# Kernel tuning notes

Measured on AMD Instinct MI355X. Metric: run time of the kernel, lower is better.

The kernel has to match this reference:

```python
import jax, jax.numpy as jnp
import numpy as np
from jax.scipy.linalg import solve_triangular

REG = 1e-3  # DCDicL regularization hyperparameter


def _p2o(psf, H, W):
    # point-spread-function -> optical transfer function: zero-pad to (H,W),
    # circularly shift so kernel center sits at origin, then rfft2.
    ds = psf.shape[-1]
    otf = jnp.zeros(psf.shape[:-2] + (H, W), psf.dtype)
    otf = otf.at[..., :ds, :ds].set(psf)
    otf = jnp.roll(otf, (-(ds // 2), -(ds // 2)), axis=(-2, -1))
    return jnp.fft.rfft2(otf)


def _solve_fft(X, D, Y, alpha, H, W):
    # X:(N,1,Cin,H,Wf)  D:(N,Cout,Cin,H,Wf)  Y:(N,Cout,1,H,Wf)  complex64
    C_in = X.shape[2]
    a = (alpha / C_in)[..., None]              # (N,1,1,1,1) real scalar per sample
    Dc = jnp.conj(D)
    Z = Y * D + a * X                          # (N,Cout,Cin,H,Wf)
    factor1 = Z / a
    num = jnp.sum(Dc * Z, axis=2, keepdims=True)
    den = a * jnp.sum(Dc * D, axis=2, keepdims=True) + a * a  # csum: real add
    factor2 = D * (num / den)
    Xn = jnp.mean(factor1 - factor2, axis=1)   # (N,Cin,H,Wf)
    return jnp.fft.irfft2(Xn, s=(H, W))


def _solve_ls(x, d, y, alpha, reg):
    # x:(N,Cin,H,W)  d:(N,Cout,Cin,ds,ds)  y:(N,Cout,H,W)
    N, C_in, H, W = x.shape
    C_out, ds = d.shape[1], d.shape[-1]
    P = ds - 1
    M = C_in * ds * ds
    dn = ('NCHW', 'OIHW', 'NCHW')

    # All-pairs full cross-correlation (torch cal_xtx via sample-wise conv3d):
    # corr[n,i,o,u,v] = sum_{h,w} x[n,i,h+u-P,w+v-P] * x[n,o,h,w]
    def pair_corr(xn):
        return jax.lax.conv_general_dilated(xn[:, None], xn[:, None], (1, 1),
                                            [(P, P), (P, P)], dimension_numbers=dn)
    corr = jax.vmap(pair_corr)(x)              # (N, i, o, 2P+1, 2P+1)

    # Block-Toeplitz Gram (replaces unfold/flip/index-permute copies):
    # Q[n,(o,k1,k2),(i,q1,q2)] = corr[n,i,o, P+q1-k1, P+q2-k2]
    r = jnp.arange(ds)
    off = P + r[None, :] - r[:, None]          # (k, q)
    Q6 = corr[:, :, :, off[:, :, None, None], off[None, None, :, :]]  # (N,i,o,k1,q1,k2,q2)
    Q = jnp.transpose(Q6, (0, 2, 3, 5, 1, 4, 6)).reshape(N, M, M)

    # cal_xty: 'same'-padded correlation of x with y
    p = (ds - 1) // 2
    def xty_corr(xn, yn):
        return jax.lax.conv_general_dilated(xn[:, None], yn[:, None], (1, 1),
                                            [(p, p), (p, p)], dimension_numbers=dn)
    xty = jax.vmap(xty_corr)(x, y)             # (N, i, Cout, ds, ds)
    Pm = jnp.transpose(xty, (0, 1, 3, 4, 2)).reshape(N, M, C_out)

    a = (alpha * (H * W) * reg / (ds * ds * C_in)).reshape(N, 1, 1)
    Q = Q + a * jnp.eye(M, dtype=Q.dtype)
    Pm = Pm + a * jnp.transpose(d.reshape(N, C_out, M), (0, 2, 1))

    L = jnp.linalg.cholesky(Q)
    Zs = solve_triangular(L, Pm, lower=True)
    Dm = solve_triangular(jnp.swapaxes(L, -1, -2), Zs, lower=False)
    return jnp.transpose(Dm.reshape(N, C_in, ds, ds, C_out), (0, 4, 1, 2, 3))


def _forward(x, d, y, alpha_x, alpha_d, reg):
    H, W = x.shape[-2], x.shape[-1]
    X = jnp.fft.rfft2(x)[:, None]              # (N,1,Cin,H,Wf)
    D = _p2o(d, H, W)                          # (N,Cout,Cin,H,Wf)
    Y = jnp.fft.rfft2(y)[:, :, None]           # (N,Cout,1,H,Wf)
    x_new = _solve_fft(X, D, Y, alpha_x, H, W)
    d_new = _solve_ls(x_new, d, y, alpha_d, reg)
    return x_new, d_new


def setup_inputs() -> dict:
    key = jax.random.key(0)
    k0, k1, k2 = jax.random.split(key, 3)
    x = jax.random.normal(k0, (4, 64, 128, 128), jnp.float32)
    d = jax.random.normal(k1, (4, 1, 64, 5, 5), jnp.float32)
    y = jax.random.normal(k2, (4, 1, 128, 128), jnp.float32)
    alpha_x = jnp.ones((4, 1, 1, 1), jnp.float32)
    alpha_d = jnp.ones((4, 1, 1, 1), jnp.float32)
    reg = jnp.float32(REG)
    return {"x": x, "d": d, "y": y, "alpha_x": alpha_x, "alpha_d": alpha_d, "reg": reg}


def reference(x, d, y, alpha_x, alpha_d, reg):
    return _forward(x, d, y, alpha_x, alpha_d, reg)
```

## Files before the change

kernel.cpp:

```cpp
#include <hip/hip_runtime.h>
#include <hip/hip_bf16.h>
#include <math.h>

#define PI_F 3.14159265358979323846f

#define NS   4
#define CIN  64
#define HH   128
#define WW   128
#define KXN  65
#define NPIX (HH*WW)
#define MMAT 1600
#define NIT  6
#define SD   136
#define SLAB 167936

#define OFF_SINV 0
#define OFF_E    33280
#define OFF_ER   98816
#define OFF_VR   231936
#define OFF_WB   298496
#define OFF_R    364032
#define OFF_RP   1691136
#define OFF_EP   1691136
#define OFF_PP   1691136
#define OFF_XB   7196160
#define XB0C     4734976
#define OFF_DV   0
#define OFF_RV   6400
#define OFF_PV   12800
#define OFF_AP   19200
#define OFF_RV2  25600
#define OFF_PAPP 32000

#define WRED(x) { (x)+=__shfl_down((x),32); (x)+=__shfl_down((x),16); (x)+=__shfl_down((x),8); \
                  (x)+=__shfl_down((x),4);  (x)+=__shfl_down((x),2);  (x)+=__shfl_down((x),1); }

typedef __attribute__((ext_vector_type(8))) short bf16x8;
typedef __attribute__((ext_vector_type(4))) float f32x4;

__global__ __launch_bounds__(256) void k_sinv(const float* __restrict__ dict,
                                              const float* __restrict__ alpha_x,
                                              float* __restrict__ ws) {
  int idx = blockIdx.x * 256 + threadIdx.x;
  int n = blockIdx.y;
  if (idx >= HH * KXN) return;
  int ky = idx / KXN, kx = idx % KXN;
  float tr[25], ti[25];
  {
    float eyr[5], eyi[5], exr[5], exi[5];
#pragma unroll
    for (int a = 0; a < 5; ++a) {
      float s, c;
      sincosf(-2.0f * PI_F * (float)(ky * (a - 2)) / 128.0f, &s, &c);
      eyr[a] = c; eyi[a] = s;
      sincosf(-2.0f * PI_F * (float)(kx * (a - 2)) / 128.0f, &s, &c);
      exr[a] = c; exi[a] = s;
    }
#pragma unroll
    for (int a = 0; a < 5; ++a)
#pragma unroll
      for (int b = 0; b < 5; ++b) {
        tr[a*5+b] = eyr[a]*exr[b] - eyi[a]*exi[b];
        ti[a*5+b] = eyr[a]*exi[b] + eyi[a]*exr[b];
      }
  }
  const float* dn = dict + n * CIN * 25;
  float S = 0.0f;
  for (int c = 0; c < CIN; ++c) {
    const float* p = dn + c * 25;
    float Dr = 0.0f, Di = 0.0f;
#pragma unroll
    for (int t = 0; t < 25; ++t) { Dr += p[t]*tr[t]; Di += p[t]*ti[t]; }
    S += Dr*Dr + Di*Di;
  }
  float a = alpha_x[n] * (1.0f/64.0f);
  ws[OFF_SINV + (n*HH + ky)*KXN + kx] = 1.0f / (S + a);
}

__global__ __launch_bounds__(256) void k_e(const float* __restrict__ x,
                                           const float* __restrict__ dict,
                                           float* __restrict__ ws) {
  __shared__ __align__(16) float xs[68*SD];
  __shared__ float psf_s[25];
  int c = blockIdx.x, n = blockIdx.y, hh = blockIdx.z;
  int tid = threadIdx.x;
  if (tid < 25) psf_s[tid] = dict[(n*CIN + c)*25 + tid];
  const float* Xc = x + (size_t)(n*CIN + c)*NPIX;
  int rbase = hh*64 - 2;
  for (int k = tid; k < 68*132; k += 256) {
    int R = k / 132, C = k - R*132;
    int gh = (rbase + R) & 127;
    int gw = (C - 2) & 127;
    xs[R*SD + C] = Xc[gh*128 + gw];
  }
  __syncthreads();
  int cs = tid & 31, rs = tid >> 5;
  int c0 = cs*4, r0 = rs*8;
  float w[5][8];
#pragma unroll
  for (int k = 0; k < 4; ++k) {
    f32x4 a = *(const f32x4*)&xs[(r0+k)*SD + c0];
    f32x4 b = *(const f32x4*)&xs[(r0+k)*SD + c0 + 4];
#pragma unroll
    for (int e = 0; e < 4; ++e) { w[k][e] = a[e]; w[k][4+e] = b[e]; }
  }
  float* EPo = ws + OFF_EP + (size_t)(c*4 + n)*NPIX + (size_t)(hh*64 + r0)*128 + c0;
#pragma unroll
  for (int row = 0; row < 8; ++row) {
    int slot = (row + 4) % 5;
    f32x4 a = *(const f32x4*)&xs[(r0+row+4)*SD + c0];
    f32x4 b = *(const f32x4*)&xs[(r0+row+4)*SD + c0 + 4];
#pragma unroll
    for (int e = 0; e < 4; ++e) { w[slot][e] = a[e]; w[slot][4+e] = b[e]; }
    f32x4 acc = (f32x4){0.f,0.f,0.f,0.f};
#pragma unroll
    for (int u = 0; u < 5; ++u)
#pragma unroll
      for (int v = 0; v < 5; ++v) {
        float pv = psf_s[u*5 + v];
#pragma unroll
        for (int p = 0; p < 4; ++p)
          acc[p] += pv * w[(row+u) % 5][p+v];
      }
    *(f32x4*)(EPo + (size_t)row*128) = acc;
  }
}

__global__ __launch_bounds__(256) void k_e2(const float* __restrict__ y,
                                            float* __restrict__ ws) {
  int n = blockIdx.y;
  int p = blockIdx.x*256 + threadIdx.x;
  float s = 0.0f;
#pragma unroll 8
  for (int c = 0; c < CIN; ++c) s += ws[OFF_EP + (size_t)(c*4 + n)*NPIX + p];
  ws[OFF_E + n*NPIX + p] = y[n*NPIX + p] - s;
}

__global__ __launch_bounds__(256) void k_fft_rows(float* __restrict__ ws) {
  __shared__ float twr[128], twi[128];
  int tid = threadIdx.x;
  if (tid < 128) { float s, c; sincosf(-2.0f*PI_F*(float)tid/128.0f, &s, &c); twr[tid]=c; twi[tid]=s; }
  __syncthreads();
  int idx = blockIdx.x*256 + tid, n = blockIdx.y;
  if (idx >= HH*KXN) return;
  int h = idx / KXN, k = idx % KXN;
  const float* row = ws + OFF_E + (n*HH + h)*WW;
  float sr = 0, si = 0;
  for (int w = 0; w < 128; ++w) {
    int t = (w*k) & 127;
    float v = row[w];
    sr += v*twr[t]; si += v*twi[t];
  }
  float* o = ws + OFF_ER + ((n*HH + h)*KXN + k)*2;
  o[0] = sr; o[1] = si;
}

__global__ __launch_bounds__(128) void k_fft_colpipe(float* __restrict__ ws) {
  __shared__ float twr[128], twi[128];
  __shared__ float ecr[128], eci[128];
  __shared__ float ewr[128], ewi[128];
  int tid = threadIdx.x;
  int kx = blockIdx.x, n = blockIdx.y;
  { float s, c; sincosf(-2.0f*PI_F*(float)tid/128.0f, &s, &c); twr[tid]=c; twi[tid]=s; }
  const float* Er = ws + OFF_ER + (size_t)n*HH*KXN*2;
  ecr[tid] = Er[(tid*KXN + kx)*2];
  eci[tid] = Er[(tid*KXN + kx)*2 + 1];
  __syncthreads();
  {
    int ky = tid;
    float sr = 0, si = 0;
    for (int h = 0; h < 128; ++h) {
      int t = (h*ky) & 127;
      float ar = ecr[h], ai = eci[h];
      sr += ar*twr[t] - ai*twi[t];
      si += ar*twi[t] + ai*twr[t];
    }
    float sv = ws[OFF_SINV + (n*HH + ky)*KXN + kx];
    ewr[ky] = sr*sv; ewi[ky] = si*sv;
  }
  __syncthreads();
  {
    int h = tid;
    float sr = 0, si = 0;
    for (int ky = 0; ky < 128; ++ky) {
      int t = (h*ky) & 127;
      float ar = ewr[ky], ai = ewi[ky];
      sr += ar*twr[t] + ai*twi[t];
      si += ai*twr[t] - ar*twi[t];
    }
    float* o = ws + OFF_VR + ((n*HH + h)*KXN + kx)*2;
    o[0] = sr; o[1] = si;
  }
}

__global__ __launch_bounds__(256) void k_ifft_rows(float* __restrict__ ws) {
  __shared__ float twr[128], twi[128];
  int tid = threadIdx.x;
  if (tid < 128) { float s, c; sincosf(-2.0f*PI_F*(float)tid/128.0f, &s, &c); twr[tid]=c; twi[tid]=s; }
  __syncthreads();
  int idx = blockIdx.x*256 + tid, n = blockIdx.y;
  int h = idx >> 7, w = idx & 127;
  const float* Vr = ws + OFF_VR + (size_t)n*HH*KXN*2;
  float s = 0.0f;
  for (int kx = 0; kx <= 64; ++kx) {
    int t = (w*kx) & 127;
    float ar = Vr[(h*KXN + kx)*2], ai = Vr[(h*KXN + kx)*2 + 1];
    float re = ar*twr[t] + ai*twi[t];
    s += (kx == 0 || kx == 64) ? re : 2.0f*re;
  }
  ws[OFF_WB + (n*HH + h)*WW + w] = s * (1.0f/16384.0f);
}

__global__ __launch_bounds__(256) void k_xnew(const float* __restrict__ x,
                                              const float* __restrict__ dict,
                                              const float* __restrict__ ws,
                                              float* __restrict__ out) {
  __shared__ float psf_s[CIN*25];
  __shared__ float wt[20*20];
  int n = blockIdx.y, tile = blockIdx.x, tid = threadIdx.x;
  int h0 = (tile >> 3) * 16, w0 = (tile & 7) * 16;
  for (int i = tid; i < CIN*25; i += 256) psf_s[i] = dict[n*CIN*25 + i];
  for (int i = tid; i < 400; i += 256) {
    int r = i / 20, cc = i % 20;
    int gh = (h0 + r - 2) & 127, gw = (w0 + cc - 2) & 127;
    wt[i] = ws[OFF_WB + (n*HH + gh)*WW + gw];
  }
  __syncthreads();
  int py = tid >> 4, px = tid & 15;
  int h = h0+py, w = w0+px;
  for (int c = 0; c < CIN; ++c) {
    float acc = 0.0f;
    const float* pp = psf_s + c*25;
#pragma unroll
    for (int a = 0; a < 5; ++a)
#pragma unroll
      for (int b = 0; b < 5; ++b)
        acc += pp[a*5+b] * wt[(py + 4 - a)*20 + (px + 4 - b)];
    int gi = ((n*CIN + c)*HH + h)*WW + w;
    out[gi] = x[gi] + acc;
  }
}

__global__ __launch_bounds__(256) void k_pad(const float* __restrict__ xn,
                                             float* __restrict__ ws) {
  ushort* xb0 = (ushort*)(ws + OFF_XB);
  ushort* xb1 = xb0 + XB0C;
  int ch = blockIdx.y;
  int idx = blockIdx.x*256 + threadIdx.x;
  if (ch == 0 && idx == 0) xb1[0] = 0;
  if (idx >= 136*136) return;
  int hp = idx / 136, wp = idx % 136;
  float v = 0.0f;
  if (hp >= 4 && hp < 132 && wp >= 4 && wp < 132)
    v = xn[(size_t)ch*NPIX + (hp-4)*128 + (wp-4)];
  __hip_bfloat16 b = __float2bfloat16(v);
  ushort bits = *(ushort*)&b;
  size_t o = (size_t)ch*18496 + idx;
  xb0[o] = bits;
  xb1[o + 1] = bits;
}

__global__ __launch_bounds__(256, 3) void k_gemm(float* __restrict__ ws) {
  __shared__ __align__(16) ushort sA0[64*128];
  __shared__ __align__(16) ushort sA1[64*128];
  __shared__ __align__(16) ushort sB [64*128];

  const ushort* xb0 = (const ushort*)(ws + OFF_XB);
  const ushort* xb1 = xb0 + XB0C;
  int fid = blockIdx.x;
  int xcd = fid & 7, l = fid >> 3;
  int nn = xcd & 3, hi = xcd >> 2;
  int g = l % 21, m = l / 21;
  int sl = m*2 + hi;

  int tid = threadIdx.x;
  int wv = tid >> 6, lane = tid & 63;
  int l16 = lane & 15, quad = lane >> 4;
  int lr = lane >> 4, lc = lane & 15;

  int sidx0 = 2*g;
  int sidx1 = 2*g + 1;
  int sval1 = (sidx1 <= 40);
  if (sidx1 > 40) sidx1 = 40;
  int uv0 = sidx0 + 40, uv1 = sidx1 + 40;
  int u0 = uv0 / 9, v0 = uv0 % 9;
  int u1 = uv1 / 9, v1 = uv1 % 9;

  size_t chanBase = (size_t)(nn*64) * 18496;
  int ridx0 = sl * 16;
  const ushort* pB  = xb0 + chanBase + 548 + (size_t)ridx0*136;
  size_t a0e = chanBase + (size_t)(u0 + ridx0)*136 + v0;
  size_t a1e = chanBase + (size_t)(u1 + ridx0)*136 + v1;
  const ushort* pA0 = (v0 & 1) ? (xb1 + a0e + 1) : (xb0 + a0e);
  const ushort* pA1 = (v1 & 1) ? (xb1 + a1e + 1) : (xb0 + a1e);

  f32x4 acc[2][4];
#pragma unroll
  for (int s = 0; s < 2; ++s)
#pragma unroll
    for (int jt = 0; jt < 4; ++jt) acc[s][jt] = (f32x4){0.f,0.f,0.f,0.f};

  for (int r = 0; r < 16; ++r) {
    if (r) __syncthreads();
#pragma unroll
    for (int c = 0; c < 4; ++c) {
      int row = wv*16 + c*4 + lr;
      int sw = ((lc ^ (row & 15)) * 8);
      size_t goff = (size_t)row * 18496 + (size_t)lc * 8;
      {
        const uint2* p = (const uint2*)(pB + goff);
        uint2 b0 = p[0], b1 = p[1];
        *(uint2*)&sB[row*128 + sw]     = b0;
        *(uint2*)&sB[row*128 + sw + 4] = b1;
      }
      {
        const uint* p = (const uint*)(pA0 + goff);
        uint4 v4; v4.x = p[0]; v4.y = p[1]; v4.z = p[2]; v4.w = p[3];
        *(uint4*)&sA0[row*128 + sw] = v4;
      }
      {
        const uint* p = (const uint*)(pA1 + goff);
        uint4 v4; v4.x = p[0]; v4.y = p[1]; v4.z = p[2]; v4.w = p[3];
        *(uint4*)&sA1[row*128 + sw] = v4;
      }
    }
    __syncthreads();
#pragma unroll
    for (int kt = 0; kt < 4; ++kt) {
      int c16 = kt*4 + quad;
      int sw = ((c16 ^ l16) * 8);
      bf16x8 af0 = *(const bf16x8*)&sA0[(wv*16 + l16)*128 + sw];
      bf16x8 af1 = *(const bf16x8*)&sA1[(wv*16 + l16)*128 + sw];
      bf16x8 bf[4];
#pragma unroll
      for (int jt = 0; jt < 4; ++jt)
        bf[jt] = *(const bf16x8*)&sB[(jt*16 + l16)*128 + sw];
#pragma unroll
      for (int jt = 0; jt < 4; ++jt) {
        acc[0][jt] = __builtin_amdgcn_mfma_f32_16x16x32_bf16(af0, bf[jt], acc[0][jt], 0, 0, 0);
        acc[1][jt] = __builtin_amdgcn_mfma_f32_16x16x32_bf16(af1, bf[jt], acc[1][jt], 0, 0, 0);
      }
    }
    pB += 136; pA0 += 136; pA1 += 136;
  }

  int io = wv*16 + quad*4;
  {
    float* dst = ws + OFF_RP + (((size_t)nn*8 + sl)*41 + sidx0)*4096;
#pragma unroll
    for (int jt = 0; jt < 4; ++jt) {
      int jout = jt*16 + l16;
      *reinterpret_cast<f32x4*>(dst + jout*64 + io) = acc[0][jt];
    }
  }
  if (sval1) {
    float* dst = ws + OFF_RP + (((size_t)nn*8 + sl)*41 + sidx1)*4096;
#pragma unroll
    for (int jt = 0; jt < 4; ++jt) {
      int jout = jt*16 + l16;
      *reinterpret_cast<f32x4*>(dst + jout*64 + io) = acc[1][jt];
    }
  }
}

__global__ __launch_bounds__(256) void k_rsumtrans(float* __restrict__ ws) {
  __shared__ float tile[64][65];
  int s = blockIdx.x, n = blockIdx.y;
  float* base0 = ws + OFF_RP + ((size_t)n*8)*SLAB + (size_t)s*4096;
  int t = threadIdx.x;
#pragma unroll
  for (int p = 0; p < 4; ++p) {
    int vidx = p*256 + t;
    int row = vidx >> 4, c0 = (vidx & 15)*4;
    f32x4 sum = (f32x4){0.f,0.f,0.f,0.f};
#pragma unroll
    for (int sl = 0; sl < 8; ++sl)
      sum += *(const f32x4*)(base0 + (size_t)sl*SLAB + row*64 + c0);
    *(f32x4*)(base0 + row*64 + c0) = sum;
    tile[row][c0]   = sum[0]; tile[row][c0+1] = sum[1];
    tile[row][c0+2] = sum[2]; tile[row][c0+3] = sum[3];
  }
  __syncthreads();
  float* PT = base0 + SLAB;
#pragma unroll
  for (int p = 0; p < 4; ++p) {
    int vidx = p*256 + t;
    int row = vidx >> 4, c0 = (vidx & 15)*4;
    f32x4 o;
#pragma unroll
    for (int e = 0; e < 4; ++e) o[e] = tile[c0+e][row];
    *(f32x4*)(PT + row*64 + c0) = o;
  }
}

__global__ __launch_bounds__(256) void k_rmerge(float* __restrict__ ws) {
  __shared__ float ld[81][65];
  int i = blockIdx.x, n = blockIdx.y;
  const float* P  = ws + OFF_RP + ((size_t)n*8 + 0)*SLAB;
  const float* PT = ws + OFF_RP + ((size_t)n*8 + 1)*SLAB;
  int t = threadIdx.x;
  for (int k = t; k < 81*64; k += 256) {
    int uv = k >> 6, j = k & 63;
    float v = (uv >= 40) ? PT[(size_t)(uv-40)*4096 + i*64 + j]
                         : P [(size_t)(40-uv)*4096 + i*64 + j];
    ld[uv][j] = v;
  }
  __syncthreads();
  float* out = ws + OFF_R + ((size_t)(n*64 + i)*64)*81;
  for (int k = t; k < 64*81; k += 256) {
    int j = k / 81, uv = k - j*81;
    out[k] = ld[uv][j];
  }
}

__global__ __launch_bounds__(256) void k_pm(const float* __restrict__ xn,
                                            const float* __restrict__ y,
                                            float* __restrict__ ws) {
  __shared__ __align__(16) float xs[68*SD];
  __shared__ float red_s[4][25];
  int i = blockIdx.x, n = blockIdx.y, hh = blockIdx.z;
  int tid = threadIdx.x;
  const float* Xi = xn + (size_t)(n*CIN + i)*NPIX;
  int rbase = hh*64 - 2;
  for (int k = tid; k < 68*132; k += 256) {
    int R = k / 132, C = k - R*132;
    int hr = rbase + R, wc = C - 2;
    float v = 0.0f;
    if (hr >= 0 && hr < 128 && wc >= 0 && wc < 128) v = Xi[hr*128 + wc];
    xs[R*SD + C] = v;
  }
  __syncthreads();
  int cs = tid & 31, rs = tid >> 5;
  int c0 = cs*4, r0 = rs*8;
  float w[5][8];
#pragma unroll
  for (int k = 0; k < 4; ++k) {
    f32x4 a = *(const f32x4*)&xs[(r0+k)*SD + c0];
    f32x4 b = *(const f32x4*)&xs[(r0+k)*SD + c0 + 4];
#pragma unroll
    for (int e = 0; e < 4; ++e) { w[k][e] = a[e]; w[k][4+e] = b[e]; }
  }
  float acc[25];
#pragma unroll
  for (int t = 0; t < 25; ++t) acc[t] = 0.0f;
  const float* yp = y + (size_t)n*NPIX + (size_t)(hh*64 + r0)*128 + c0;
#pragma unroll
  for (int row = 0; row < 8; ++row) {
    int slot = (row + 4) % 5;
    f32x4 a = *(const f32x4*)&xs[(r0+row+4)*SD + c0];
    f32x4 b = *(const f32x4*)&xs[(r0+row+4)*SD + c0 + 4];
#pragma unroll
    for (int e = 0; e < 4; ++e) { w[slot][e] = a[e]; w[slot][4+e] = b[e]; }
    f32x4 yv = *(const f32x4*)(yp + (size_t)row*128);
#pragma unroll
    for (int u = 0; u < 5; ++u)
#pragma unroll
      for (int v = 0; v < 5; ++v) {
#pragma unroll
        for (int p = 0; p < 4; ++p)
          acc[u*5+v] += w[(row+u) % 5][p+v] * yv[p];
      }
  }
  int lane = tid & 63, wv = tid >> 6;
#pragma unroll
  for (int t = 0; t < 25; ++t) {
    float v = acc[t];
    WRED(v);
    if (lane == 0) red_s[wv][t] = v;
  }
  __syncthreads();
  if (tid < 25) {
    float s = red_s[0][tid] + red_s[1][tid] + red_s[2][tid] + red_s[3][tid];
    ws[OFF_PP + ((size_t)(hh*4 + n)*64 + i)*25 + tid] = s;
  }
}

__global__ __launch_bounds__(64) void k_pm2(const float* __restrict__ dict,
                                            const float* __restrict__ alpha_d,
                                            const float* __restrict__ regp,
                                            float* __restrict__ ws) {
  int i = blockIdx.x, n = blockIdx.y, t = threadIdx.x;
  if (t >= 25) return;
  float s = 0.0f;
#pragma unroll
  for (int tg = 0; tg < 2; ++tg) s += ws[OFF_PP + ((size_t)(tg*4 + n)*64 + i)*25 + t];
  float ad = alpha_d[n] * 16384.0f * regp[0] * (1.0f/1600.0f);
  float val = s + ad * dict[(n*CIN + i)*25 + t];
  int idx = n*MMAT + i*25 + t;
  ws[OFF_RV + idx] = val;
  ws[OFF_PV + idx] = val;
}

__global__ __launch_bounds__(256) void k_cg_first(float* __restrict__ ws,
                                                  const float* __restrict__ alpha_d,
                                                  const float* __restrict__ regp) {
  __shared__ float vv[MMAT];
  __shared__ float part[25][66];
  int n = blockIdx.y, j = blockIdx.x, tid = threadIdx.x;
  for (int t = tid; t < MMAT; t += 256) vv[t] = ws[OFF_PV + n*MMAT + t];
  __syncthreads();
  int i = tid & 63, qq = tid >> 6;
  const float* Rij = ws + OFF_R + (((size_t)n*CIN + i)*CIN + j)*81;
  const float* vi = &vv[i*25];
#pragma unroll
  for (int s6 = 0; s6 < 7; ++s6) {
    int ac = qq + 4*s6;
    if (ac < 25) {
      int a = ac/5, c = ac%5;
      float s = 0.0f;
#pragma unroll
      for (int b = 0; b < 5; ++b)
#pragma unroll
        for (int d = 0; d < 5; ++d)
          s += Rij[(4+b-a)*9 + (4+d-c)] * vi[b*5+d];
      part[ac][i] = s;
    }
  }
  __syncthreads();
  float contrib = 0.0f;
  if (tid < 25) {
    float s = 0.0f;
    for (int t = 0; t < 64; ++t) s += part[tid][t];
    float reg = alpha_d[n] * 16384.0f * regp[0] * (1.0f/1600.0f);
    s += reg * vv[j*25 + tid];
    ws[OFF_AP + n*MMAT + j*25 + tid] = s;
    contrib = s * vv[j*25 + tid];
  }
  if (tid < 64) {
    WRED(contrib);
    if (tid == 0) ws[OFF_PAPP + 0*256 + n*64 + j] = contrib;
  }
}

__global__ __launch_bounds__(256) void k_cg_step(float* __restrict__ ws, int it,
                                                 int last, float* __restrict__ out,
                                                 const float* __restrict__ alpha_d,
                                                 const float* __restrict__ regp) {
  __shared__ float vv[MMAT];
  __shared__ float red_s[9];
  __shared__ float part[25][66];
  int n = blockIdx.y, j = blockIdx.x, tid = threadIdx.x;
  const float* rsrc = ws + ((it & 1) ? OFF_RV2 : OFF_RV) + n*MMAT;
  float*       rdst = ws + ((it & 1) ? OFF_RV  : OFF_RV2) + n*MMAT;
  int lane = tid & 63, wvi = tid >> 6;

  float rold[7], apv[7];
  float rrp = 0.0f;
#pragma unroll
  for (int t = 0; t < 7; ++t) {
    int idx = tid + 256*t;
    rold[t] = 0.0f; apv[t] = 0.0f;
    if (idx < MMAT) {
      rold[t] = rsrc[idx];
      apv[t]  = ws[OFF_AP + n*MMAT + idx];
      rrp += rold[t]*rold[t];
    }
  }
  WRED(rrp);
  if (lane == 0) red_s[wvi] = rrp;
  float pp = (tid < 64) ? ws[OFF_PAPP + it*256 + n*64 + tid] : 0.0f;
  if (tid < 64) { WRED(pp); if (tid == 0) red_s[4] = pp; }
  __syncthreads();
  float rr_old = red_s[0] + red_s[1] + red_s[2] + red_s[3];
  float alpha = rr_old / (red_s[4] + 1e-30f);

  if (last) {
    if (tid < 25) {
      int idx = n*MMAT + j*25 + tid;
      float dv = ws[OFF_DV + idx] + alpha * ws[OFF_PV + idx];
      out[4194304 + n*MMAT + j*25 + tid] = dv;
    }
    return;
  }

  float rrnp = 0.0f;
#pragma unroll
  for (int t = 0; t < 7; ++t) {
    int idx = tid + 256*t;
    if (idx < MMAT) {
      float rn = rold[t] - alpha * apv[t];
      vv[idx] = rn;
      rrnp += rn*rn;
    }
  }
  WRED(rrnp);
  __syncthreads();
  if (lane == 0) red_s[5 + wvi] = rrnp;
  __syncthreads();
  float rr_new = red_s[5] + red_s[6] + red_s[7] + red_s[8];
  float beta = rr_new / (rr_old + 1e-30f);

  int i = tid & 63, qq = tid >> 6;
  const float* Rij = ws + OFF_R + (((size_t)n*CIN + i)*CIN + j)*81;
  const float* vi = &vv[i*25];
#pragma unroll
  for (int s6 = 0; s6 < 7; ++s6) {
    int ac = qq + 4*s6;
    if (ac < 25) {
      int a = ac/5, c = ac%5;
      float s = 0.0f;
#pragma unroll
      for (int b = 0; b < 5; ++b)
#pragma unroll
        for (int d = 0; d < 5; ++d)
          s += Rij[(4+b-a)*9 + (4+d-c)] * vi[b*5+d];
      part[ac][i] = s;
    }
  }
  __syncthreads();
  float contrib = 0.0f;
  if (tid < 25) {
    float s = 0.0f;
    for (int t = 0; t < 64; ++t) s += part[tid][t];
    float reg = alpha_d[n] * 16384.0f * regp[0] * (1.0f/1600.0f);
    float rn_seg = vv[j*25 + tid];
    s += reg * rn_seg;
    int idx = n*MMAT + j*25 + tid;
    float p_old = ws[OFF_PV + idx];
    float dv = ws[OFF_DV + idx] + alpha * p_old;
    float pn  = rn_seg + beta * p_old;
    float apn = s + beta * ws[OFF_AP + idx];
    ws[OFF_DV + idx] = dv;
    ws[OFF_PV + idx] = pn;
    ws[OFF_AP + idx] = apn;
    rdst[j*25 + tid] = rn_seg;
    contrib = pn * apn;
  }
  if (tid < 64) {
    WRED(contrib);
    if (tid == 0) ws[OFF_PAPP + (it+1)*256 + n*64 + j] = contrib;
  }
}

extern "C" void kernel_launch(void* const* d_in, const int* in_sizes, int n_in,
                              void* d_out, int out_size, void* d_ws, size_t ws_size,
                              hipStream_t stream) {
  (void)in_sizes; (void)n_in; (void)out_size; (void)ws_size;
  const float* x    = (const float*)d_in[0];
  const float* dict = (const float*)d_in[1];
  const float* y    = (const float*)d_in[2];
  const float* ax   = (const float*)d_in[3];
  const float* ad   = (const float*)d_in[4];
  const float* regp = (const float*)d_in[5];
  float* out = (float*)d_out;
  float* ws  = (float*)d_ws;

  dim3 b256(256);
  k_sinv<<<dim3(33,4), b256, 0, stream>>>(dict, ax, ws);
  k_e<<<dim3(64,4,2), b256, 0, stream>>>(x, dict, ws);
  k_e2<<<dim3(64,4), b256, 0, stream>>>(y, ws);
  k_fft_rows<<<dim3(33,4), b256, 0, stream>>>(ws);
  k_fft_colpipe<<<dim3(65,4), dim3(128), 0, stream>>>(ws);
  k_ifft_rows<<<dim3(64,4), b256, 0, stream>>>(ws);
  k_xnew<<<dim3(64,4), b256, 0, stream>>>(x, dict, ws, out);

  k_pad<<<dim3(73,256), b256, 0, stream>>>(out, ws);
  k_gemm<<<dim3(672), b256, 0, stream>>>(ws);
  k_rsumtrans<<<dim3(41,4), b256, 0, stream>>>(ws);
  k_rmerge<<<dim3(64,4), b256, 0, stream>>>(ws);

  k_pm<<<dim3(64,4,2), b256, 0, stream>>>(out, y, ws);
  k_pm2<<<dim3(64,4), dim3(64), 0, stream>>>(dict, ad, regp, ws);

  k_cg_first<<<dim3(64,4), b256, 0, stream>>>(ws, ad, regp);
  for (int it = 0; it < NIT; ++it)
    k_cg_step<<<dim3(64,4), b256, 0, stream>>>(ws, it, (it == NIT-1) ? 1 : 0, out, ad, regp);
}
```

Baseline: 315.8 us.

## Double-buffer GEMM LDS tiles with register prefetch and transpose R layout for coalescing

```diff
diff --git a/kernel.cpp b/kernel.cpp
--- a/kernel.cpp
+++ b/kernel.cpp
@@ -262,9 +262,9 @@
 }
 
 __global__ __launch_bounds__(256, 3) void k_gemm(float* __restrict__ ws) {
-  __shared__ __align__(16) ushort sA0[64*128];
-  __shared__ __align__(16) ushort sA1[64*128];
-  __shared__ __align__(16) ushort sB [64*128];
+  __shared__ __align__(16) ushort sA0[2][64*64];
+  __shared__ __align__(16) ushort sA1[2][64*64];
+  __shared__ __align__(16) ushort sB [2][64*64];
 
   const ushort* xb0 = (const ushort*)(ws + OFF_XB);
   const ushort* xb1 = xb0 + XB0C;
@@ -277,7 +277,6 @@
   int tid = threadIdx.x;
   int wv = tid >> 6, lane = tid & 63;
   int l16 = lane & 15, quad = lane >> 4;
-  int lr = lane >> 4, lc = lane & 15;
 
   int sidx0 = 2*g;
   int sidx1 = 2*g + 1;
@@ -289,11 +288,22 @@
 
   size_t chanBase = (size_t)(nn*64) * 18496;
   int ridx0 = sl * 16;
-  const ushort* pB  = xb0 + chanBase + 548 + (size_t)ridx0*136;
+  const ushort* pBb = xb0 + chanBase + 548 + (size_t)ridx0*136;
   size_t a0e = chanBase + (size_t)(u0 + ridx0)*136 + v0;
   size_t a1e = chanBase + (size_t)(u1 + ridx0)*136 + v1;
-  const ushort* pA0 = (v0 & 1) ? (xb1 + a0e + 1) : (xb0 + a0e);
-  const ushort* pA1 = (v1 & 1) ? (xb1 + a1e + 1) : (xb0 + a1e);
+  const ushort* pA0b = (v0 & 1) ? (xb1 + a0e + 1) : (xb0 + a0e);
+  const ushort* pA1b = (v1 & 1) ? (xb1 + a1e + 1) : (xb0 + a1e);
+
+  int srow = tid >> 2;
+  int scc0 = (tid & 3) * 2;
+  size_t sgoff = (size_t)srow * 18496 + (size_t)scc0 * 8;
+  int swz0 = (scc0 ^ (srow & 7)) * 8;
+  int swz1 = ((scc0+1) ^ (srow & 7)) * 8;
+  int wbase = srow * 64;
+
+  auto rv = [&](int r2)->size_t {
+    return (size_t)(r2 >> 1) * 136 + (size_t)(r2 & 1) * 64;
+  };
 
   f32x4 acc[2][4];
 #pragma unroll
@@ -301,48 +311,60 @@
 #pragma unroll
     for (int jt = 0; jt < 4; ++jt) acc[s][jt] = (f32x4){0.f,0.f,0.f,0.f};
 
-  for (int r = 0; r < 16; ++r) {
-    if (r) __syncthreads();
-#pragma unroll
-    for (int c = 0; c < 4; ++c) {
-      int row = wv*16 + c*4 + lr;
-      int sw = ((lc ^ (row & 15)) * 8);
-      size_t goff = (size_t)row * 18496 + (size_t)lc * 8;
-      {
-        const uint2* p = (const uint2*)(pB + goff);
-        uint2 b0 = p[0], b1 = p[1];
-        *(uint2*)&sB[row*128 + sw]     = b0;
-        *(uint2*)&sB[row*128 + sw + 4] = b1;
-      }
-      {
-        const uint* p = (const uint*)(pA0 + goff);
-        uint4 v4; v4.x = p[0]; v4.y = p[1]; v4.z = p[2]; v4.w = p[3];
-        *(uint4*)&sA0[row*128 + sw] = v4;
-      }
-      {
-        const uint* p = (const uint*)(pA1 + goff);
-        uint4 v4; v4.x = p[0]; v4.y = p[1]; v4.z = p[2]; v4.w = p[3];
-        *(uint4*)&sA1[row*128 + sw] = v4;
-      }
-    }
-    __syncthreads();
-#pragma unroll
-    for (int kt = 0; kt < 4; ++kt) {
-      int c16 = kt*4 + quad;
-      int sw = ((c16 ^ l16) * 8);
-      bf16x8 af0 = *(const bf16x8*)&sA0[(wv*16 + l16)*128 + sw];
-      bf16x8 af1 = *(const bf16x8*)&sA1[(wv*16 + l16)*128 + sw];
+  uint2 rB[4]; uint rA0[8], rA1[8];
+  auto load_round = [&](int r2) {
+    size_t d = rv(r2) + sgoff;
+    const uint2* pb = (const uint2*)(pBb + d);
+#pragma unroll
+    for (int q = 0; q < 4; ++q) rB[q] = pb[q];
+    const uint* pa0 = (const uint*)(pA0b + d);
+#pragma unroll
+    for (int q = 0; q < 8; ++q) rA0[q] = pa0[q];
+    const uint* pa1 = (const uint*)(pA1b + d);
+#pragma unroll
+    for (int q = 0; q < 8; ++q) rA1[q] = pa1[q];
+  };
+  auto write_round = [&](int buf) {
+    uint4 vb0 = make_uint4(rB[0].x, rB[0].y, rB[1].x, rB[1].y);
+    uint4 vb1 = make_uint4(rB[2].x, rB[2].y, rB[3].x, rB[3].y);
+    *(uint4*)&sB[buf][wbase + swz0] = vb0;
+    *(uint4*)&sB[buf][wbase + swz1] = vb1;
+    uint4 va00 = make_uint4(rA0[0], rA0[1], rA0[2], rA0[3]);
+    uint4 va01 = make_uint4(rA0[4], rA0[5], rA0[6], rA0[7]);
+    *(uint4*)&sA0[buf][wbase + swz0] = va00;
+    *(uint4*)&sA0[buf][wbase + swz1] = va01;
+    uint4 va10 = make_uint4(rA1[0], rA1[1], rA1[2], rA1[3]);
+    uint4 va11 = make_uint4(rA1[4], rA1[5], rA1[6], rA1[7]);
+    *(uint4*)&sA1[buf][wbase + swz0] = va10;
+    *(uint4*)&sA1[buf][wbase + swz1] = va11;
+  };
+
+  load_round(0);
+  write_round(0);
+  __syncthreads();
+
+  int cur = 0;
+  for (int r2 = 0; r2 < 32; ++r2) {
+    if (r2 < 31) load_round(r2 + 1);
+#pragma unroll
+    for (int kt2 = 0; kt2 < 2; ++kt2) {
+      int cc = kt2*4 + quad;
+      int swz = ((cc ^ (l16 & 7)) * 8);
+      bf16x8 af0 = *(const bf16x8*)&sA0[cur][(wv*16 + l16)*64 + swz];
+      bf16x8 af1 = *(const bf16x8*)&sA1[cur][(wv*16 + l16)*64 + swz];
       bf16x8 bf[4];
 #pragma unroll
       for (int jt = 0; jt < 4; ++jt)
-        bf[jt] = *(const bf16x8*)&sB[(jt*16 + l16)*128 + sw];
+        bf[jt] = *(const bf16x8*)&sB[cur][(jt*16 + l16)*64 + swz];
 #pragma unroll
       for (int jt = 0; jt < 4; ++jt) {
         acc[0][jt] = __builtin_amdgcn_mfma_f32_16x16x32_bf16(af0, bf[jt], acc[0][jt], 0, 0, 0);
         acc[1][jt] = __builtin_amdgcn_mfma_f32_16x16x32_bf16(af1, bf[jt], acc[1][jt], 0, 0, 0);
       }
     }
-    pB += 136; pA0 += 136; pA1 += 136;
+    if (r2 < 31) write_round(cur ^ 1);
+    __syncthreads();
+    cur ^= 1;
   }
 
   int io = wv*16 + quad*4;
@@ -395,22 +417,16 @@
 }
 
 __global__ __launch_bounds__(256) void k_rmerge(float* __restrict__ ws) {
-  __shared__ float ld[81][65];
-  int i = blockIdx.x, n = blockIdx.y;
+  int j = blockIdx.x, n = blockIdx.y;
   const float* P  = ws + OFF_RP + ((size_t)n*8 + 0)*SLAB;
   const float* PT = ws + OFF_RP + ((size_t)n*8 + 1)*SLAB;
+  float* out = ws + OFF_R + ((size_t)(n*64 + j))*81*64;
   int t = threadIdx.x;
   for (int k = t; k < 81*64; k += 256) {
-    int uv = k >> 6, j = k & 63;
-    float v = (uv >= 40) ? PT[(size_t)(uv-40)*4096 + i*64 + j]
-                         : P [(size_t)(40-uv)*4096 + i*64 + j];
-    ld[uv][j] = v;
-  }
-  __syncthreads();
-  float* out = ws + OFF_R + ((size_t)(n*64 + i)*64)*81;
-  for (int k = t; k < 64*81; k += 256) {
-    int j = k / 81, uv = k - j*81;
-    out[k] = ld[uv][j];
+    int uv = k >> 6, i = k & 63;
+    float v = (uv >= 40) ? P [(size_t)(uv-40)*4096 + j*64 + i]
+                         : PT[(size_t)(40-uv)*4096 + j*64 + i];
+    out[k] = v;
   }
 }
 
@@ -501,7 +517,7 @@
   for (int t = tid; t < MMAT; t += 256) vv[t] = ws[OFF_PV + n*MMAT + t];
   __syncthreads();
   int i = tid & 63, qq = tid >> 6;
-  const float* Rij = ws + OFF_R + (((size_t)n*CIN + i)*CIN + j)*81;
+  const float* Rj = ws + OFF_R + ((size_t)(n*CIN + j))*81*64;
   const float* vi = &vv[i*25];
 #pragma unroll
   for (int s6 = 0; s6 < 7; ++s6) {
@@ -513,7 +529,7 @@
       for (int b = 0; b < 5; ++b)
 #pragma unroll
         for (int d = 0; d < 5; ++d)
-          s += Rij[(4+b-a)*9 + (4+d-c)] * vi[b*5+d];
+          s += Rj[((4+b-a)*9 + (4+d-c))*64 + i] * vi[b*5+d];
       part[ac][i] = s;
     }
   }
@@ -592,7 +608,7 @@
   float beta = rr_new / (rr_old + 1e-30f);
 
   int i = tid & 63, qq = tid >> 6;
-  const float* Rij = ws + OFF_R + (((size_t)n*CIN + i)*CIN + j)*81;
+  const float* Rj = ws + OFF_R + ((size_t)(n*CIN + j))*81*64;
   const float* vi = &vv[i*25];
 #pragma unroll
   for (int s6 = 0; s6 < 7; ++s6) {
@@ -604,7 +620,7 @@
       for (int b = 0; b < 5; ++b)
 #pragma unroll
         for (int d = 0; d < 5; ++d)
-          s += Rij[(4+b-a)*9 + (4+d-c)] * vi[b*5+d];
+          s += Rj[((4+b-a)*9 + (4+d-c))*64 + i] * vi[b*5+d];
       part[ac][i] = s;
     }
   }
```

Result: faster. 299.2 us (-5.2%).

## Retile x_new convolution per channel and transpose R layout for coalesced CG reads

Applied to the files above, without the earlier changes.

```diff
diff --git a/kernel.cpp b/kernel.cpp
--- a/kernel.cpp
+++ b/kernel.cpp
@@ -216,29 +216,50 @@
                                               const float* __restrict__ dict,
                                               const float* __restrict__ ws,
                                               float* __restrict__ out) {
-  __shared__ float psf_s[CIN*25];
-  __shared__ float wt[20*20];
-  int n = blockIdx.y, tile = blockIdx.x, tid = threadIdx.x;
-  int h0 = (tile >> 3) * 16, w0 = (tile & 7) * 16;
-  for (int i = tid; i < CIN*25; i += 256) psf_s[i] = dict[n*CIN*25 + i];
-  for (int i = tid; i < 400; i += 256) {
-    int r = i / 20, cc = i % 20;
-    int gh = (h0 + r - 2) & 127, gw = (w0 + cc - 2) & 127;
-    wt[i] = ws[OFF_WB + (n*HH + gh)*WW + gw];
-  }
-  __syncthreads();
-  int py = tid >> 4, px = tid & 15;
-  int h = h0+py, w = w0+px;
-  for (int c = 0; c < CIN; ++c) {
-    float acc = 0.0f;
-    const float* pp = psf_s + c*25;
-#pragma unroll
-    for (int a = 0; a < 5; ++a)
-#pragma unroll
-      for (int b = 0; b < 5; ++b)
-        acc += pp[a*5+b] * wt[(py + 4 - a)*20 + (px + 4 - b)];
-    int gi = ((n*CIN + c)*HH + h)*WW + w;
-    out[gi] = x[gi] + acc;
+  __shared__ __align__(16) float xs[68*SD];
+  __shared__ float psf_s[25];
+  int c = blockIdx.x, n = blockIdx.y, hh = blockIdx.z;
+  int tid = threadIdx.x;
+  if (tid < 25) psf_s[tid] = dict[(n*CIN + c)*25 + 24 - tid];
+  const float* Wb = ws + OFF_WB + (size_t)n*NPIX;
+  int rbase = hh*64 - 2;
+  for (int k = tid; k < 68*132; k += 256) {
+    int R = k / 132, C = k - R*132;
+    int gh = (rbase + R) & 127;
+    int gw = (C - 2) & 127;
+    xs[R*SD + C] = Wb[gh*128 + gw];
+  }
+  __syncthreads();
+  int cs = tid & 31, rs = tid >> 5;
+  int c0 = cs*4, r0 = rs*8;
+  float w[5][8];
+#pragma unroll
+  for (int k = 0; k < 4; ++k) {
+    f32x4 a = *(const f32x4*)&xs[(r0+k)*SD + c0];
+    f32x4 b = *(const f32x4*)&xs[(r0+k)*SD + c0 + 4];
+#pragma unroll
+    for (int e = 0; e < 4; ++e) { w[k][e] = a[e]; w[k][4+e] = b[e]; }
+  }
+  const float* Xc = x   + (size_t)(n*CIN + c)*NPIX + (size_t)(hh*64 + r0)*128 + c0;
+  float*       Oc = out + (size_t)(n*CIN + c)*NPIX + (size_t)(hh*64 + r0)*128 + c0;
+#pragma unroll
+  for (int row = 0; row < 8; ++row) {
+    int slot = (row + 4) % 5;
+    f32x4 a = *(const f32x4*)&xs[(r0+row+4)*SD + c0];
+    f32x4 b = *(const f32x4*)&xs[(r0+row+4)*SD + c0 + 4];
+#pragma unroll
+    for (int e = 0; e < 4; ++e) { w[slot][e] = a[e]; w[slot][4+e] = b[e]; }
+    f32x4 acc = *(const f32x4*)(Xc + (size_t)row*128);
+#pragma unroll
+    for (int u = 0; u < 5; ++u)
+#pragma unroll
+      for (int v = 0; v < 5; ++v) {
+        float pv = psf_s[u*5 + v];
+#pragma unroll
+        for (int p = 0; p < 4; ++p)
+          acc[p] += pv * w[(row+u) % 5][p+v];
+      }
+    *(f32x4*)(Oc + (size_t)row*128) = acc;
   }
 }
 
@@ -395,22 +416,16 @@
 }
 
 __global__ __launch_bounds__(256) void k_rmerge(float* __restrict__ ws) {
-  __shared__ float ld[81][65];
-  int i = blockIdx.x, n = blockIdx.y;
+  int j = blockIdx.x, n = blockIdx.y;
   const float* P  = ws + OFF_RP + ((size_t)n*8 + 0)*SLAB;
   const float* PT = ws + OFF_RP + ((size_t)n*8 + 1)*SLAB;
+  float* out = ws + OFF_R + ((size_t)(n*64 + j))*81*64;
   int t = threadIdx.x;
   for (int k = t; k < 81*64; k += 256) {
-    int uv = k >> 6, j = k & 63;
-    float v = (uv >= 40) ? PT[(size_t)(uv-40)*4096 + i*64 + j]
-                         : P [(size_t)(40-uv)*4096 + i*64 + j];
-    ld[uv][j] = v;
-  }
-  __syncthreads();
-  float* out = ws + OFF_R + ((size_t)(n*64 + i)*64)*81;
-  for (int k = t; k < 64*81; k += 256) {
-    int j = k / 81, uv = k - j*81;
-    out[k] = ld[uv][j];
+    int uv = k >> 6, i = k & 63;
+    float v = (uv >= 40) ? P [(size_t)(uv-40)*4096 + j*64 + i]
+                         : PT[(size_t)(40-uv)*4096 + j*64 + i];
+    out[k] = v;
   }
 }
 
@@ -501,7 +516,7 @@
   for (int t = tid; t < MMAT; t += 256) vv[t] = ws[OFF_PV + n*MMAT + t];
   __syncthreads();
   int i = tid & 63, qq = tid >> 6;
-  const float* Rij = ws + OFF_R + (((size_t)n*CIN + i)*CIN + j)*81;
+  const float* Rj = ws + OFF_R + ((size_t)(n*CIN + j))*81*64;
   const float* vi = &vv[i*25];
 #pragma unroll
   for (int s6 = 0; s6 < 7; ++s6) {
@@ -513,7 +528,7 @@
       for (int b = 0; b < 5; ++b)
 #pragma unroll
         for (int d = 0; d < 5; ++d)
-          s += Rij[(4+b-a)*9 + (4+d-c)] * vi[b*5+d];
+          s += Rj[((4+b-a)*9 + (4+d-c))*64 + i] * vi[b*5+d];
       part[ac][i] = s;
     }
   }
@@ -592,7 +607,7 @@
   float beta = rr_new / (rr_old + 1e-30f);
 
   int i = tid & 63, qq = tid >> 6;
-  const float* Rij = ws + OFF_R + (((size_t)n*CIN + i)*CIN + j)*81;
+  const float* Rj = ws + OFF_R + ((size_t)(n*CIN + j))*81*64;
   const float* vi = &vv[i*25];
 #pragma unroll
   for (int s6 = 0; s6 < 7; ++s6) {
@@ -604,7 +619,7 @@
       for (int b = 0; b < 5; ++b)
 #pragma unroll
         for (int d = 0; d < 5; ++d)
-          s += Rij[(4+b-a)*9 + (4+d-c)] * vi[b*5+d];
+          s += Rj[((4+b-a)*9 + (4+d-c))*64 + i] * vi[b*5+d];
       part[ac][i] = s;
     }
   }
@@ -653,7 +668,7 @@
   k_fft_rows<<<dim3(33,4), b256, 0, stream>>>(ws);
   k_fft_colpipe<<<dim3(65,4), dim3(128), 0, stream>>>(ws);
   k_ifft_rows<<<dim3(64,4), b256, 0, stream>>>(ws);
-  k_xnew<<<dim3(64,4), b256, 0, stream>>>(x, dict, ws, out);
+  k_xnew<<<dim3(64,4,2), b256, 0, stream>>>(x, dict, ws, out);
 
   k_pad<<<dim3(73,256), b256, 0, stream>>>(out, ws);
   k_gemm<<<dim3(672), b256, 0, stream>>>(ws);
```

After: 272.4 us. 13.7% less time.
